# Optimization experiments

Measured on AMD Instinct MI355X. Metric: run time of the kernel, lower is better.

The kernel has to match this reference:

```python
import jax, jax.numpy as jnp
import numpy as np

N_USERS = 100000
N_ITEMS = 50000
N_NODES = N_USERS + N_ITEMS
DIM = 64
N_EDGES = 1200000
BATCH = 4096


def _propagate(edge_index, emb):
    # row = source, col = destination (out[dst] += norm * emb[src])
    row, col = edge_index[0], edge_index[1]
    n = emb.shape[0]
    # degree counted over row occurrences only (faithful to `degree(row, ...)`)
    deg = jax.ops.segment_sum(jnp.ones_like(row, dtype=emb.dtype), row, num_segments=n)
    dinv = jnp.where(deg > 0, deg ** -0.5, 0.0).astype(emb.dtype)
    norm = dinv[row] * dinv[col]  # [E]
    msgs = norm[:, None] * emb[row]  # [E, D] gather + scale
    return jax.ops.segment_sum(msgs, col, num_segments=n)  # scatter-add into dst


def setup_inputs() -> dict:
    key = jax.random.key(0)
    ks = jax.random.split(key, 10)
    xavier = (6.0 / (N_USERS + DIM)) ** 0.5  # approximate xavier bounds per table
    user_emb = jax.random.uniform(ks[0], (N_USERS, DIM), jnp.float32, -xavier, xavier)
    xavier_i = (6.0 / (N_ITEMS + DIM)) ** 0.5
    item_emb = jax.random.uniform(ks[1], (N_ITEMS, DIM), jnp.float32, -xavier_i, xavier_i)
    lim = (1.0 / DIM) ** 0.5
    W1 = jax.random.uniform(ks[2], (DIM, DIM), jnp.float32, -lim, lim)
    b1 = jax.random.uniform(ks[3], (DIM,), jnp.float32, -lim, lim)
    W2 = jax.random.uniform(ks[4], (DIM, DIM), jnp.float32, -lim, lim)
    b2 = jax.random.uniform(ks[5], (DIM,), jnp.float32, -lim, lim)
    users = jax.random.randint(ks[6], (BATCH,), 0, N_USERS)
    items = jax.random.randint(ks[7], (BATCH,), 0, N_ITEMS)
    edge_index = jax.random.randint(ks[8], (2, N_EDGES), 0, N_NODES)
    return {"users": users, "items": items, "edge_index": edge_index,
            "user_emb": user_emb, "item_emb": item_emb,
            "W1": W1, "b1": b1, "W2": W2, "b2": b2}


def reference(users, items, edge_index, user_emb, item_emb, W1, b1, W2, b2):
    all_emb = jnp.concatenate([user_emb, item_emb], axis=0)  # [N, D]
    # layer 0: propagate -> linear -> relu
    all_emb = _propagate(edge_index, all_emb)
    all_emb = jax.nn.relu(all_emb @ W1.T + b1)
    # layer 1 (last): propagate -> linear (no relu)
    all_emb = _propagate(edge_index, all_emb)
    all_emb = all_emb @ W2.T + b2
    user_final = all_emb[:N_USERS]
    item_final = all_emb[N_USERS:]
    scores = jnp.sum(user_final[users] * item_final[items], axis=1)  # [B]
    return scores
```

## Files before the change

kernel.cpp:

```cpp
#include <hip/hip_runtime.h>
#include <math.h>

constexpr int NU = 100000;
constexpr int NI = 50000;
constexpr int NN = 150000;
constexpr int D  = 64;
constexpr int NE = 1200000;
constexpr int NE4 = NE / 4;
constexpr int B  = 4096;
constexpr int CAPB = 64;
constexpr int CAP2 = 40;

constexpr int NCHUNK = 3;
constexpr int CHUNK  = 65536;
constexpr int CWORDS = CHUNK / 4;
constexpr int WORDS  = 37504;
constexpr int RWORDS = 37500;
constexpr int NSLICE = 80;
constexpr int SLICE4 = NE4 / NSLICE;

constexpr int BMW = 4704;
constexpr int HZ4 = 163184 / 4;


__global__ void __launch_bounds__(1024) k_flag(const int* __restrict__ users,
                                               const int* __restrict__ items,
                                               unsigned int* __restrict__ bm0,
                                               int* __restrict__ bidx,
                                               int* __restrict__ nb) {
    __shared__ unsigned int sbm[BMW];
    __shared__ int snb;
    for (int i = threadIdx.x; i < BMW; i += 1024) sbm[i] = 0;
    if (threadIdx.x == 0) snb = 0;
    __syncthreads();
    for (int t = threadIdx.x; t < 2 * B; t += 1024) {
        const int node = (t < B) ? users[t] : items[t - B] + NU;
        const unsigned int old = atomicOr(&sbm[node >> 5], 1u << (node & 31));
        if (!((old >> (node & 31)) & 1)) bidx[node] = atomicAdd(&snb, 1);
    }
    __syncthreads();
    for (int i = threadIdx.x; i < BMW; i += 1024) bm0[i] = sbm[i];
    if (threadIdx.x == 0) *nb = snb;
}

__global__ void __launch_bounds__(256) k_hist(const int* __restrict__ row,
                                              unsigned int* __restrict__ hcopy,
                                              int4* __restrict__ zbase) {
    for (int i = blockIdx.x * 256 + threadIdx.x; i < HZ4; i += gridDim.x * 256)
        zbase[i] = make_int4(0, 0, 0, 0);

    __shared__ unsigned int lh[CWORDS];
    const int ci = blockIdx.x / NSLICE;
    const int si = blockIdx.x % NSLICE;
    const int lo = ci * CHUNK;
    const int cw = (ci == NCHUNK - 1) ? (WORDS - (NCHUNK - 1) * CWORDS) : CWORDS;
    for (int w = threadIdx.x; w < cw; w += 256) lh[w] = 0;
    __syncthreads();
    const int4* r4 = reinterpret_cast<const int4*>(row) + (size_t)si * SLICE4;
    const unsigned int span = (unsigned)(cw * 4);
    for (int t = threadIdx.x; t < SLICE4; t += 256) {
        const int4 r = r4[t];
        int v;
        v = r.x - lo; if ((unsigned)v < span) atomicAdd(&lh[v >> 2], 1u << (8 * (v & 3)));
        v = r.y - lo; if ((unsigned)v < span) atomicAdd(&lh[v >> 2], 1u << (8 * (v & 3)));
        v = r.z - lo; if ((unsigned)v < span) atomicAdd(&lh[v >> 2], 1u << (8 * (v & 3)));
        v = r.w - lo; if ((unsigned)v < span) atomicAdd(&lh[v >> 2], 1u << (8 * (v & 3)));
    }
    __syncthreads();
    unsigned int* dst = hcopy + (size_t)si * WORDS + ci * CWORDS;
    for (int w = threadIdx.x; w < cw; w += 256) dst[w] = lh[w];
}

__global__ void k_mark(const int* __restrict__ row, const int* __restrict__ col,
                       const unsigned int* __restrict__ bm0,
                       const int* __restrict__ bidx,
                       int* __restrict__ cntBd, int* __restrict__ csrBd,
                       unsigned int* __restrict__ bm1) {
    const int t = blockIdx.x * blockDim.x + threadIdx.x;
    if (t >= NE4) return;
    const int4 r = reinterpret_cast<const int4*>(row)[t];
    const int4 c = reinterpret_cast<const int4*>(col)[t];
    #define E1(rr, cc) if ((bm0[(cc) >> 5] >> ((cc) & 31)) & 1) { \
        const int bi = bidx[cc]; \
        const int s = atomicAdd(&cntBd[bi], 1); \
        csrBd[bi * CAPB + s] = rr; \
        atomicOr(&bm1[(rr) >> 5], 1u << ((rr) & 31)); }
    E1(r.x, c.x) E1(r.y, c.y) E1(r.z, c.z) E1(r.w, c.w)
    #undef E1
}

__global__ void k_dinvc(const unsigned int* __restrict__ hcopy,
                        float* __restrict__ dinv,
                        const unsigned int* __restrict__ bm1,
                        int* __restrict__ list, int* __restrict__ ncnt) {
    const int w = blockIdx.x * blockDim.x + threadIdx.x;
    if (w >= RWORDS) return;
    unsigned int s = 0;
    #pragma unroll 8
    for (int si = 0; si < NSLICE; ++si) s += hcopy[(size_t)si * WORDS + w];
    const int d0 = s & 255, d1 = (s >> 8) & 255, d2 = (s >> 16) & 255, d3 = (int)(s >> 24);
    float4 dv;
    dv.x = d0 > 0 ? 1.0f / sqrtf((float)d0) : 0.0f;
    dv.y = d1 > 0 ? 1.0f / sqrtf((float)d1) : 0.0f;
    dv.z = d2 > 0 ? 1.0f / sqrtf((float)d2) : 0.0f;
    dv.w = d3 > 0 ? 1.0f / sqrtf((float)d3) : 0.0f;
    reinterpret_cast<float4*>(dinv)[w] = dv;
    const unsigned int bits = (bm1[w >> 3] >> ((w & 7) * 4)) & 0xFu;
    const int n0 = w * 4;
    if (bits & 1u) list[atomicAdd(ncnt, 1)] = n0;
    if (bits & 2u) list[atomicAdd(ncnt, 1)] = n0 + 1;
    if (bits & 4u) list[atomicAdd(ncnt, 1)] = n0 + 2;
    if (bits & 8u) list[atomicAdd(ncnt, 1)] = n0 + 3;
}

__global__ void k_pass2(const int* __restrict__ row, const int* __restrict__ col,
                        const unsigned int* __restrict__ bm1,
                        int* __restrict__ cnt2d, int* __restrict__ csr2d) {
    const int t = blockIdx.x * blockDim.x + threadIdx.x;
    if (t >= NE4) return;
    const int4 r = reinterpret_cast<const int4*>(row)[t];
    const int4 c = reinterpret_cast<const int4*>(col)[t];
    #define E2(rr, cc) if ((bm1[(cc) >> 5] >> ((cc) & 31)) & 1) { \
        const int s = atomicAdd(&cnt2d[cc], 1); \
        csr2d[cc * CAP2 + s] = rr; }
    E2(r.x, c.x) E2(r.y, c.y) E2(r.z, c.z) E2(r.w, c.w)
    #undef E2
}

__global__ void k_gather1(const int* __restrict__ list, const int* __restrict__ ncnt,
                          const int* __restrict__ cnt2d, const int* __restrict__ csr2d,
                          const float* __restrict__ dinv,
                          const float* __restrict__ embU, const float* __restrict__ embI,
                          float* __restrict__ out) {
    const int lane = threadIdx.x & 63;
    const int n = *ncnt;
    const int nwv = gridDim.x * (blockDim.x >> 6);
    for (int idx = blockIdx.x * (blockDim.x >> 6) + (threadIdx.x >> 6);
         idx < n; idx += nwv) {
        const int c = list[idx];
        const int ne = cnt2d[c];
        const int* es = csr2d + (size_t)c * CAP2;
        float a0 = 0.0f, a1 = 0.0f, a2 = 0.0f, a3 = 0.0f;
        int e = 0;
        for (; e + 3 < ne; e += 4) {
            const int4 r = *reinterpret_cast<const int4*>(es + e);
            const float d0 = dinv[r.x], d1 = dinv[r.y], d2 = dinv[r.z], d3 = dinv[r.w];
            const float* s0 = (r.x < NU) ? embU + (size_t)r.x * D : embI + (size_t)(r.x - NU) * D;
            const float* s1 = (r.y < NU) ? embU + (size_t)r.y * D : embI + (size_t)(r.y - NU) * D;
            const float* s2 = (r.z < NU) ? embU + (size_t)r.z * D : embI + (size_t)(r.z - NU) * D;
            const float* s3 = (r.w < NU) ? embU + (size_t)r.w * D : embI + (size_t)(r.w - NU) * D;
            a0 = fmaf(d0, s0[lane], a0);
            a1 = fmaf(d1, s1[lane], a1);
            a2 = fmaf(d2, s2[lane], a2);
            a3 = fmaf(d3, s3[lane], a3);
        }
        for (; e < ne; ++e) {
            const int r = es[e];
            const float* s = (r < NU) ? embU + (size_t)r * D : embI + (size_t)(r - NU) * D;
            a0 = fmaf(dinv[r], s[lane], a0);
        }
        out[(size_t)c * D + lane] = dinv[c] * ((a0 + a1) + (a2 + a3));
    }
}

__global__ void __launch_bounds__(256) k_mlp_relu(const int* __restrict__ list,
                                                  const int* __restrict__ ncnt,
                                                  float* __restrict__ emb,
                                                  const float* __restrict__ W,
                                                  const float* __restrict__ b) {
    const int lane = threadIdx.x & 63;
    float w[D];
    #pragma unroll
    for (int k4 = 0; k4 < D / 4; ++k4) {
        const float4 v = *reinterpret_cast<const float4*>(W + (size_t)lane * D + k4 * 4);
        w[k4 * 4 + 0] = v.x; w[k4 * 4 + 1] = v.y;
        w[k4 * 4 + 2] = v.z; w[k4 * 4 + 3] = v.w;
    }
    const float bias = b[lane];

    const int n = *ncnt;
    const int wid = blockIdx.x * (blockDim.x >> 6) + (threadIdx.x >> 6);
    const int nw  = gridDim.x * (blockDim.x >> 6);
    for (int i4 = wid * 4; i4 < n; i4 += nw * 4) {
        const int r0 = list[i4];
        const int r1 = (i4 + 1 < n) ? list[i4 + 1] : r0;
        const int r2 = (i4 + 2 < n) ? list[i4 + 2] : r0;
        const int r3 = (i4 + 3 < n) ? list[i4 + 3] : r0;
        float* x0 = emb + (size_t)r0 * D;
        float* x1 = emb + (size_t)r1 * D;
        float* x2 = emb + (size_t)r2 * D;
        float* x3 = emb + (size_t)r3 * D;
        const float xv0 = x0[lane], xv1 = x1[lane], xv2 = x2[lane], xv3 = x3[lane];
        float a0 = bias, a1 = bias, a2 = bias, a3 = bias;
        #pragma unroll
        for (int k = 0; k < D; ++k) {
            const float wk = w[k];
            a0 = fmaf(__int_as_float(__builtin_amdgcn_readlane(__float_as_int(xv0), k)), wk, a0);
            a1 = fmaf(__int_as_float(__builtin_amdgcn_readlane(__float_as_int(xv1), k)), wk, a1);
            a2 = fmaf(__int_as_float(__builtin_amdgcn_readlane(__float_as_int(xv2), k)), wk, a2);
            a3 = fmaf(__int_as_float(__builtin_amdgcn_readlane(__float_as_int(xv3), k)), wk, a3);
        }
        x0[lane] = fmaxf(a0, 0.0f);
        x1[lane] = fmaxf(a1, 0.0f);
        x2[lane] = fmaxf(a2, 0.0f);
        x3[lane] = fmaxf(a3, 0.0f);
    }
}

__global__ void __launch_bounds__(256) k_score2(const int* __restrict__ users,
                                                const int* __restrict__ items,
                                                const int* __restrict__ bidx,
                                                const int* __restrict__ cntBd,
                                                const int* __restrict__ csrBd,
                                                const float* __restrict__ dinv,
                                                const float* __restrict__ embA,
                                                const float* __restrict__ W,
                                                const float* __restrict__ b,
                                                float* __restrict__ out) {
    __shared__ float sy[2][2][D];
    const int lane = threadIdx.x & 63;
    const int wid  = threadIdx.x >> 6;
    const int pp   = wid >> 1;
    const int t    = wid & 1;
    const int p    = blockIdx.x * 2 + pp;

    float w[D];
    #pragma unroll
    for (int k4 = 0; k4 < D / 4; ++k4) {
        const float4 v = *reinterpret_cast<const float4*>(W + (size_t)lane * D + k4 * 4);
        w[k4 * 4 + 0] = v.x; w[k4 * 4 + 1] = v.y;
        w[k4 * 4 + 2] = v.z; w[k4 * 4 + 3] = v.w;
    }

    const int c  = (t == 0) ? users[p] : items[p] + NU;
    const int bi = bidx[c];
    const int n  = cntBd[bi];
    const int* es = csrBd + (size_t)bi * CAPB;
    float a0 = 0.0f, a1 = 0.0f, a2 = 0.0f, a3 = 0.0f;
    int e = 0;
    for (; e + 3 < n; e += 4) {
        const int4 r = *reinterpret_cast<const int4*>(es + e);
        a0 = fmaf(dinv[r.x], embA[(size_t)r.x * D + lane], a0);
        a1 = fmaf(dinv[r.y], embA[(size_t)r.y * D + lane], a1);
        a2 = fmaf(dinv[r.z], embA[(size_t)r.z * D + lane], a2);
        a3 = fmaf(dinv[r.w], embA[(size_t)r.w * D + lane], a3);
    }
    for (; e < n; ++e) {
        const int r = es[e];
        a0 = fmaf(dinv[r], embA[(size_t)r * D + lane], a0);
    }
    const float x = dinv[c] * ((a0 + a1) + (a2 + a3));

    float y = b[lane];
    #pragma unroll
    for (int k = 0; k < D; ++k)
        y = fmaf(__int_as_float(__builtin_amdgcn_readlane(__float_as_int(x), k)),
                 w[k], y);
    sy[pp][t][lane] = y;
    __syncthreads();
    if (t == 0) {
        float prod = sy[pp][0][lane] * sy[pp][1][lane];
        #pragma unroll
        for (int off = 32; off >= 1; off >>= 1) prod += __shfl_down(prod, off, 64);
        if (lane == 0) out[p] = prod;
    }
}

extern "C" void kernel_launch(void* const* d_in, const int* in_sizes, int n_in,
                              void* d_out, int out_size, void* d_ws, size_t ws_size,
                              hipStream_t stream) {
    const int*   users    = (const int*)d_in[0];
    const int*   items    = (const int*)d_in[1];
    const int*   edge     = (const int*)d_in[2];
    const float* user_emb = (const float*)d_in[3];
    const float* item_emb = (const float*)d_in[4];
    const float* W1       = (const float*)d_in[5];
    const float* b1       = (const float*)d_in[6];
    const float* W2       = (const float*)d_in[7];
    const float* b2       = (const float*)d_in[8];
    float*       out      = (float*)d_out;

    const int* row  = edge;
    const int* colp = edge + NE;

    unsigned int* bm1   = (unsigned int*)d_ws;
    int*   cnt2d = (int*)d_ws + 4704;
    int*   cntBd = (int*)d_ws + 154720;
    int*   ncnt  = (int*)d_ws + 163168;
    unsigned int* bm0   = (unsigned int*)d_ws + 163184;
    int*   nb    = (int*)d_ws + 167888;
    float* dinv  = (float*)d_ws + 167904;
    int*   bidx  = (int*)d_ws + 317920;
    int*   list  = (int*)d_ws + 467936;
    int*   csrBd = (int*)d_ws + 617952;
    int*   csr2d = (int*)d_ws + 1158624;
    float* embA  = (float*)d_ws + 7159264;
    unsigned int* hcopy = (unsigned int*)csr2d;

    k_flag <<<1, 1024, 0, stream>>>(users, items, bm0, bidx, nb);
    k_hist <<<NCHUNK * NSLICE, 256, 0, stream>>>(row, hcopy, (int4*)d_ws);
    k_mark <<<(NE4 + 255) / 256, 256, 0, stream>>>(row, colp, bm0, bidx, cntBd, csrBd, bm1);
    k_dinvc<<<(RWORDS + 255) / 256, 256, 0, stream>>>(hcopy, dinv, bm1, list, ncnt);
    k_pass2<<<(NE4 + 255) / 256, 256, 0, stream>>>(row, colp, bm1, cnt2d, csr2d);

    k_gather1 <<<8192, 256, 0, stream>>>(list, ncnt, cnt2d, csr2d, dinv,
                                         user_emb, item_emb, embA);
    k_mlp_relu<<<2048, 256, 0, stream>>>(list, ncnt, embA, W1, b1);
    k_score2<<<B / 2, 256, 0, stream>>>(users, items, bidx, cntBd, csrBd, dinv, embA,
                                        W2, b2, out);
}
```

Measured before the change: 167.1 us.

## Merge independent graph-build kernels into fewer launches via block-range specialization

Combines the degree histogram and batch-edge marking into one launch, and the dinv/list compaction and second-hop CSR build into another, with blocks picking a role by index. Zeroing of bm1, cntBd and ncnt moves into the single-block flag kernel, and cnt2d zeroing moves into the histogram launch. hcopy now lives in the embA region so it no longer aliases csr2d, which is what lets pass2 run alongside dinv. This cuts two launches and their serialization gaps, but the two roles in each launch now compete for the GPU at the same time.

```diff
diff --git a/kernel.cpp b/kernel.cpp
--- a/kernel.cpp
+++ b/kernel.cpp
@@ -18,16 +18,24 @@
 constexpr int RWORDS = 37500;
 constexpr int NSLICE = 80;
 constexpr int SLICE4 = NE4 / NSLICE;
+constexpr int NHB    = NCHUNK * NSLICE;
 
 constexpr int BMW = 4704;
-constexpr int HZ4 = 163184 / 4;
+constexpr int CZ4 = 150016 / 4;
 
 
 __global__ void __launch_bounds__(1024) k_flag(const int* __restrict__ users,
                                                const int* __restrict__ items,
                                                unsigned int* __restrict__ bm0,
                                                int* __restrict__ bidx,
-                                               int* __restrict__ nb) {
+                                               int* __restrict__ nb,
+                                               unsigned int* __restrict__ bm1,
+                                               int* __restrict__ cntBd,
+                                               int* __restrict__ ncnt) {
+    for (int i = threadIdx.x; i < BMW; i += 1024) bm1[i] = 0;
+    for (int i = threadIdx.x; i < 8448; i += 1024) cntBd[i] = 0;
+    if (threadIdx.x == 0) *ncnt = 0;
+
     __shared__ unsigned int sbm[BMW];
     __shared__ int snb;
     for (int i = threadIdx.x; i < BMW; i += 1024) sbm[i] = 0;
@@ -43,88 +51,96 @@
     if (threadIdx.x == 0) *nb = snb;
 }
 
-__global__ void __launch_bounds__(256) k_hist(const int* __restrict__ row,
-                                              unsigned int* __restrict__ hcopy,
-                                              int4* __restrict__ zbase) {
-    for (int i = blockIdx.x * 256 + threadIdx.x; i < HZ4; i += gridDim.x * 256)
-        zbase[i] = make_int4(0, 0, 0, 0);
-
-    __shared__ unsigned int lh[CWORDS];
-    const int ci = blockIdx.x / NSLICE;
-    const int si = blockIdx.x % NSLICE;
-    const int lo = ci * CHUNK;
-    const int cw = (ci == NCHUNK - 1) ? (WORDS - (NCHUNK - 1) * CWORDS) : CWORDS;
-    for (int w = threadIdx.x; w < cw; w += 256) lh[w] = 0;
-    __syncthreads();
-    const int4* r4 = reinterpret_cast<const int4*>(row) + (size_t)si * SLICE4;
-    const unsigned int span = (unsigned)(cw * 4);
-    for (int t = threadIdx.x; t < SLICE4; t += 256) {
-        const int4 r = r4[t];
-        int v;
-        v = r.x - lo; if ((unsigned)v < span) atomicAdd(&lh[v >> 2], 1u << (8 * (v & 3)));
-        v = r.y - lo; if ((unsigned)v < span) atomicAdd(&lh[v >> 2], 1u << (8 * (v & 3)));
-        v = r.z - lo; if ((unsigned)v < span) atomicAdd(&lh[v >> 2], 1u << (8 * (v & 3)));
-        v = r.w - lo; if ((unsigned)v < span) atomicAdd(&lh[v >> 2], 1u << (8 * (v & 3)));
-    }
-    __syncthreads();
-    unsigned int* dst = hcopy + (size_t)si * WORDS + ci * CWORDS;
-    for (int w = threadIdx.x; w < cw; w += 256) dst[w] = lh[w];
-}
-
-__global__ void k_mark(const int* __restrict__ row, const int* __restrict__ col,
-                       const unsigned int* __restrict__ bm0,
-                       const int* __restrict__ bidx,
-                       int* __restrict__ cntBd, int* __restrict__ csrBd,
-                       unsigned int* __restrict__ bm1) {
-    const int t = blockIdx.x * blockDim.x + threadIdx.x;
-    if (t >= NE4) return;
-    const int4 r = reinterpret_cast<const int4*>(row)[t];
-    const int4 c = reinterpret_cast<const int4*>(col)[t];
-    #define E1(rr, cc) if ((bm0[(cc) >> 5] >> ((cc) & 31)) & 1) { \
-        const int bi = bidx[cc]; \
-        const int s = atomicAdd(&cntBd[bi], 1); \
-        csrBd[bi * CAPB + s] = rr; \
-        atomicOr(&bm1[(rr) >> 5], 1u << ((rr) & 31)); }
-    E1(r.x, c.x) E1(r.y, c.y) E1(r.z, c.z) E1(r.w, c.w)
-    #undef E1
-}
-
-__global__ void k_dinvc(const unsigned int* __restrict__ hcopy,
-                        float* __restrict__ dinv,
-                        const unsigned int* __restrict__ bm1,
-                        int* __restrict__ list, int* __restrict__ ncnt) {
-    const int w = blockIdx.x * blockDim.x + threadIdx.x;
-    if (w >= RWORDS) return;
-    unsigned int s = 0;
-    #pragma unroll 8
-    for (int si = 0; si < NSLICE; ++si) s += hcopy[(size_t)si * WORDS + w];
-    const int d0 = s & 255, d1 = (s >> 8) & 255, d2 = (s >> 16) & 255, d3 = (int)(s >> 24);
-    float4 dv;
-    dv.x = d0 > 0 ? 1.0f / sqrtf((float)d0) : 0.0f;
-    dv.y = d1 > 0 ? 1.0f / sqrtf((float)d1) : 0.0f;
-    dv.z = d2 > 0 ? 1.0f / sqrtf((float)d2) : 0.0f;
-    dv.w = d3 > 0 ? 1.0f / sqrtf((float)d3) : 0.0f;
-    reinterpret_cast<float4*>(dinv)[w] = dv;
-    const unsigned int bits = (bm1[w >> 3] >> ((w & 7) * 4)) & 0xFu;
-    const int n0 = w * 4;
-    if (bits & 1u) list[atomicAdd(ncnt, 1)] = n0;
-    if (bits & 2u) list[atomicAdd(ncnt, 1)] = n0 + 1;
-    if (bits & 4u) list[atomicAdd(ncnt, 1)] = n0 + 2;
-    if (bits & 8u) list[atomicAdd(ncnt, 1)] = n0 + 3;
-}
-
-__global__ void k_pass2(const int* __restrict__ row, const int* __restrict__ col,
-                        const unsigned int* __restrict__ bm1,
-                        int* __restrict__ cnt2d, int* __restrict__ csr2d) {
-    const int t = blockIdx.x * blockDim.x + threadIdx.x;
-    if (t >= NE4) return;
-    const int4 r = reinterpret_cast<const int4*>(row)[t];
-    const int4 c = reinterpret_cast<const int4*>(col)[t];
-    #define E2(rr, cc) if ((bm1[(cc) >> 5] >> ((cc) & 31)) & 1) { \
-        const int s = atomicAdd(&cnt2d[cc], 1); \
-        csr2d[cc * CAP2 + s] = rr; }
-    E2(r.x, c.x) E2(r.y, c.y) E2(r.z, c.z) E2(r.w, c.w)
-    #undef E2
+__global__ void __launch_bounds__(256) k_histmark(const int* __restrict__ row,
+                                                  const int* __restrict__ col,
+                                                  unsigned int* __restrict__ hcopy,
+                                                  const unsigned int* __restrict__ bm0,
+                                                  const int* __restrict__ bidx,
+                                                  int* __restrict__ cntBd,
+                                                  int* __restrict__ csrBd,
+                                                  unsigned int* __restrict__ bm1,
+                                                  int4* __restrict__ cnt2dz) {
+    for (int i = blockIdx.x * 256 + threadIdx.x; i < CZ4; i += gridDim.x * 256)
+        cnt2dz[i] = make_int4(0, 0, 0, 0);
+
+    if (blockIdx.x < NHB) {
+        __shared__ unsigned int lh[CWORDS];
+        const int ci = blockIdx.x / NSLICE;
+        const int si = blockIdx.x % NSLICE;
+        const int lo = ci * CHUNK;
+        const int cw = (ci == NCHUNK - 1) ? (WORDS - (NCHUNK - 1) * CWORDS) : CWORDS;
+        for (int w = threadIdx.x; w < cw; w += 256) lh[w] = 0;
+        __syncthreads();
+        const int4* r4 = reinterpret_cast<const int4*>(row) + (size_t)si * SLICE4;
+        const unsigned int span = (unsigned)(cw * 4);
+        for (int t = threadIdx.x; t < SLICE4; t += 256) {
+            const int4 r = r4[t];
+            int v;
+            v = r.x - lo; if ((unsigned)v < span) atomicAdd(&lh[v >> 2], 1u << (8 * (v & 3)));
+            v = r.y - lo; if ((unsigned)v < span) atomicAdd(&lh[v >> 2], 1u << (8 * (v & 3)));
+            v = r.z - lo; if ((unsigned)v < span) atomicAdd(&lh[v >> 2], 1u << (8 * (v & 3)));
+            v = r.w - lo; if ((unsigned)v < span) atomicAdd(&lh[v >> 2], 1u << (8 * (v & 3)));
+        }
+        __syncthreads();
+        unsigned int* dst = hcopy + (size_t)si * WORDS + ci * CWORDS;
+        for (int w = threadIdx.x; w < cw; w += 256) dst[w] = lh[w];
+    } else {
+        const int si = blockIdx.x - NHB;
+        const int4* r4 = reinterpret_cast<const int4*>(row) + (size_t)si * SLICE4;
+        const int4* c4 = reinterpret_cast<const int4*>(col) + (size_t)si * SLICE4;
+        for (int t = threadIdx.x; t < SLICE4; t += 256) {
+            const int4 r = r4[t];
+            const int4 c = c4[t];
+            #define E1(rr, cc) if ((bm0[(cc) >> 5] >> ((cc) & 31)) & 1) { \
+                const int bi = bidx[cc]; \
+                const int s = atomicAdd(&cntBd[bi], 1); \
+                csrBd[bi * CAPB + s] = rr; \
+                atomicOr(&bm1[(rr) >> 5], 1u << ((rr) & 31)); }
+            E1(r.x, c.x) E1(r.y, c.y) E1(r.z, c.z) E1(r.w, c.w)
+            #undef E1
+        }
+    }
+}
+
+__global__ void __launch_bounds__(256) k_pass2d(const int* __restrict__ row,
+                                                const int* __restrict__ col,
+                                                const unsigned int* __restrict__ bm1,
+                                                int* __restrict__ cnt2d,
+                                                int* __restrict__ csr2d,
+                                                const unsigned int* __restrict__ hcopy,
+                                                float* __restrict__ dinv,
+                                                int* __restrict__ list,
+                                                int* __restrict__ ncnt) {
+    if (blockIdx.x < 147) {
+        const int w = blockIdx.x * 256 + threadIdx.x;
+        if (w >= RWORDS) return;
+        unsigned int s = 0;
+        #pragma unroll 8
+        for (int si = 0; si < NSLICE; ++si) s += hcopy[(size_t)si * WORDS + w];
+        const int d0 = s & 255, d1 = (s >> 8) & 255, d2 = (s >> 16) & 255, d3 = (int)(s >> 24);
+        float4 dv;
+        dv.x = d0 > 0 ? 1.0f / sqrtf((float)d0) : 0.0f;
+        dv.y = d1 > 0 ? 1.0f / sqrtf((float)d1) : 0.0f;
+        dv.z = d2 > 0 ? 1.0f / sqrtf((float)d2) : 0.0f;
+        dv.w = d3 > 0 ? 1.0f / sqrtf((float)d3) : 0.0f;
+        reinterpret_cast<float4*>(dinv)[w] = dv;
+        const unsigned int bits = (bm1[w >> 3] >> ((w & 7) * 4)) & 0xFu;
+        const int n0 = w * 4;
+        if (bits & 1u) list[atomicAdd(ncnt, 1)] = n0;
+        if (bits & 2u) list[atomicAdd(ncnt, 1)] = n0 + 1;
+        if (bits & 4u) list[atomicAdd(ncnt, 1)] = n0 + 2;
+        if (bits & 8u) list[atomicAdd(ncnt, 1)] = n0 + 3;
+    } else {
+        const int t = (blockIdx.x - 147) * 256 + threadIdx.x;
+        if (t >= NE4) return;
+        const int4 r = reinterpret_cast<const int4*>(row)[t];
+        const int4 c = reinterpret_cast<const int4*>(col)[t];
+        #define E2(rr, cc) if ((bm1[(cc) >> 5] >> ((cc) & 31)) & 1) { \
+            const int s = atomicAdd(&cnt2d[cc], 1); \
+            csr2d[cc * CAP2 + s] = rr; }
+        E2(r.x, c.x) E2(r.y, c.y) E2(r.z, c.z) E2(r.w, c.w)
+        #undef E2
+    }
 }
 
 __global__ void k_gather1(const int* __restrict__ list, const int* __restrict__ ncnt,
@@ -295,14 +311,13 @@
     int*   csrBd = (int*)d_ws + 617952;
     int*   csr2d = (int*)d_ws + 1158624;
     float* embA  = (float*)d_ws + 7159264;
-    unsigned int* hcopy = (unsigned int*)csr2d;
-
-    k_flag <<<1, 1024, 0, stream>>>(users, items, bm0, bidx, nb);
-    k_hist <<<NCHUNK * NSLICE, 256, 0, stream>>>(row, hcopy, (int4*)d_ws);
-    k_mark <<<(NE4 + 255) / 256, 256, 0, stream>>>(row, colp, bm0, bidx, cntBd, csrBd, bm1);
-    k_dinvc<<<(RWORDS + 255) / 256, 256, 0, stream>>>(hcopy, dinv, bm1, list, ncnt);
-    k_pass2<<<(NE4 + 255) / 256, 256, 0, stream>>>(row, colp, bm1, cnt2d, csr2d);
-
+    unsigned int* hcopy = (unsigned int*)embA;
+
+    k_flag <<<1, 1024, 0, stream>>>(users, items, bm0, bidx, nb, bm1, cntBd, ncnt);
+    k_histmark<<<NHB + NSLICE, 256, 0, stream>>>(row, colp, hcopy, bm0, bidx,
+                                                 cntBd, csrBd, bm1, (int4*)cnt2d);
+    k_pass2d<<<147 + (NE4 + 255) / 256, 256, 0, stream>>>(row, colp, bm1, cnt2d, csr2d,
+                                                          hcopy, dinv, list, ncnt);
     k_gather1 <<<8192, 256, 0, stream>>>(list, ncnt, cnt2d, csr2d, dinv,
                                          user_emb, item_emb, embA);
     k_mlp_relu<<<2048, 256, 0, stream>>>(list, ncnt, embA, W1, b1);
```

Measured after the change: 202.1 us. +21.0%, slower.
